# Kernel optimization log

Measured on AMD Instinct MI355X. Metric: run time of the kernel, lower is better.

The kernel has to match this reference:

```python
import jax, jax.numpy as jnp
import numpy as np

LAYER_SIZES = [1024, 1024, 1024, 1024, 1024, 1024, 512]
MAX_PATHS = 128
BATCH = 128
N_LAYERS = len(LAYER_SIZES) - 1


def setup_inputs() -> dict:
    key = jax.random.key(0)
    keys = jax.random.split(key, 1 + 2 * N_LAYERS)
    inp = {"x": jax.random.normal(keys[0], (BATCH, LAYER_SIZES[0]), dtype=jnp.float32)}
    for i in range(N_LAYERS):
        inp[f"W{i}"] = jax.random.normal(keys[1 + 2 * i], (LAYER_SIZES[i], LAYER_SIZES[i + 1]), dtype=jnp.float32) * 0.01
        inp[f"b{i}"] = jax.random.normal(keys[2 + 2 * i], (LAYER_SIZES[i + 1],), dtype=jnp.float32) * 0.01
    return inp


def _layer(data, W, b):
    # data: [B, in_feat, P] -> [B, out_feat, 3P]
    B, _, P = data.shape
    O = W.shape[1]
    pos = jnp.einsum('bfp,fo->bpo', data, W) + b          # [B, P, O]; neg branch is exactly -pos
    branches = jnp.stack([-pos, jnp.zeros_like(pos), pos], axis=-1)  # [B, P, O, 3]
    # transpose(1,2) then reshape: interleave branches per source path, matching torch
    return branches.transpose(0, 2, 1, 3).reshape(B, O, P * 3)


def _prune(data, keep):
    # keep top-`keep` paths by L2 norm over the feature dim
    norms = jnp.linalg.norm(data, axis=1)                 # [B, P]
    _, idx = jax.lax.top_k(norms, keep)                   # [B, keep]
    return jnp.take_along_axis(data, idx[:, None, :], axis=-1)


def _forward(x, Ws, bs):
    data = x[:, :, None]                                   # [B, F, 1]
    for i in range(N_LAYERS):
        data = _layer(data, Ws[i], bs[i])
        if i < N_LAYERS - 1:
            data = jnp.tanh(data)
        if data.shape[-1] > MAX_PATHS:
            data = _prune(data, MAX_PATHS)
    # collapse with 'max_abs': per (batch, feature) pick path with largest |value|
    idx = jnp.argmax(jnp.abs(data), axis=-1, keepdims=True)
    output = jnp.take_along_axis(data, idx, axis=-1).squeeze(-1)
    return output, data


def reference(x, W0, b0, W1, b1, W2, b2, W3, b3, W4, b4, W5, b5):
    Ws = [W0, W1, W2, W3, W4, W5]
    bs = [b0, b1, b2, b3, b4, b5]
    return _forward(x, Ws, bs)
```

## Files before the change

### kernel.cpp

```cpp
#include <hip/hip_runtime.h>
#include <math.h>


using s8v = __attribute__((ext_vector_type(8))) short;
using f4v = __attribute__((ext_vector_type(4))) float;

__device__ __forceinline__ float bf2f(short b) {
  unsigned u = ((unsigned)(unsigned short)b) << 16;
  return __builtin_bit_cast(float, u);
}
__device__ __forceinline__ short f2bf(float f) {
  unsigned u = __builtin_bit_cast(unsigned, f);
  u = (u + 0x7FFFu + ((u >> 16) & 1u)) >> 16;
  return (short)u;
}
__device__ __forceinline__ void split_store(float f, short* hi, short* lo) {
  short h = f2bf(f);
  *hi = h;
  *lo = f2bf(f - bf2f(h));
}

__global__ void __launch_bounds__(256)
packx_k(const float* __restrict__ x, short* __restrict__ hi,
        short* __restrict__ lo) {
  int i = (blockIdx.x * 256 + threadIdx.x) * 4;
  float4 v = *(const float4*)&x[i];
  short4 h, l;
  h.x = f2bf(v.x); l.x = f2bf(v.x - bf2f(h.x));
  h.y = f2bf(v.y); l.y = f2bf(v.y - bf2f(h.y));
  h.z = f2bf(v.z); l.z = f2bf(v.z - bf2f(h.z));
  h.w = f2bf(v.w); l.w = f2bf(v.w - bf2f(h.w));
  *(short4*)&hi[i] = h;
  *(short4*)&lo[i] = l;
}

struct TWArgs {
  const float* W[6];
  short* Th[6];
  short* Tl[6];
};
__global__ void __launch_bounds__(256)
transW_all(TWArgs a) {
  const int z = blockIdx.z;
  const int N = (z == 5) ? 512 : 1024;
  const int n0 = blockIdx.x * 64, k0 = blockIdx.y * 64;
  if (n0 >= N) return;
  const float* __restrict__ W = a.W[z];
  short* __restrict__ Th = a.Th[z];
  short* __restrict__ Tl = a.Tl[z];
  __shared__ float tile[64][65];
  const int t = threadIdx.x;
  const int r = t >> 4, c4 = (t & 15) * 4;
#pragma unroll
  for (int i = 0; i < 4; ++i) {
    int rr = r + 16 * i;
    float4 v = *(const float4*)&W[(size_t)(k0 + rr) * N + n0 + c4];
    tile[rr][c4 + 0] = v.x;
    tile[rr][c4 + 1] = v.y;
    tile[rr][c4 + 2] = v.z;
    tile[rr][c4 + 3] = v.w;
  }
  __syncthreads();
#pragma unroll
  for (int i = 0; i < 4; ++i) {
    int n = r + 16 * i;
    short4 h, l;
    float f0 = tile[c4 + 0][n], f1 = tile[c4 + 1][n];
    float f2 = tile[c4 + 2][n], f3 = tile[c4 + 3][n];
    h.x = f2bf(f0); l.x = f2bf(f0 - bf2f(h.x));
    h.y = f2bf(f1); l.y = f2bf(f1 - bf2f(h.y));
    h.z = f2bf(f2); l.z = f2bf(f2 - bf2f(h.z));
    h.w = f2bf(f3); l.w = f2bf(f3 - bf2f(h.w));
    size_t o = (size_t)(n0 + n) * 1024 + k0 + c4;
    *(short4*)&Th[o] = h;
    *(short4*)&Tl[o] = l;
  }
}

template <int MODE, int D, int KS>
__global__ void __launch_bounds__(256, 2)
mfma_gemm(const short* __restrict__ Ah, const short* __restrict__ Al,
          const short* __restrict__ Bh, const short* __restrict__ Bl,
          const float* __restrict__ bias, short* __restrict__ Oh,
          short* __restrict__ Ol, float* __restrict__ Of, int N, int Dn) {
  constexpr int KC = 1024 / KS;
  constexpr int BKP = 40;
  __shared__ short As_h[64 * BKP], As_l[64 * BKP];
  __shared__ short Bs_h[64 * BKP], Bs_l[64 * BKP];
  const int t = threadIdx.x;
  const int row0 = blockIdx.y * 64;
  const int col0 = blockIdx.x * 64;
  const int kb = blockIdx.z * KC;
  const int sr = t >> 2, sko = (t & 3) * 8;
  const short* Ahp = Ah + (size_t)(row0 + sr) * 1024 + kb + sko;
  const short* Alp = Al + (size_t)(row0 + sr) * 1024 + kb + sko;
  const short* Bhp = Bh + (size_t)(col0 + sr) * 1024 + kb + sko;
  const short* Blp = Bl + (size_t)(col0 + sr) * 1024 + kb + sko;
  const int w = t >> 6, lane = t & 63;
  const int l16 = lane & 15, q = lane >> 4;
  const int wm0 = (w & 1) * 32, wn0 = (w >> 1) * 32;
  const int abase = (wm0 + l16) * BKP + q * 8;
  const int bbase = (wn0 + l16) * BKP + q * 8;
  f4v acc[2][2];
#pragma unroll
  for (int i = 0; i < 2; ++i)
#pragma unroll
    for (int j = 0; j < 2; ++j) acc[i][j] = (f4v){0.f, 0.f, 0.f, 0.f};
  uint4 rah = *(const uint4*)(Ahp);
  uint4 ral = *(const uint4*)(Alp);
  uint4 rbh = *(const uint4*)(Bhp);
  uint4 rbl = *(const uint4*)(Blp);
  for (int k0 = 0; k0 < KC; k0 += 32) {
    __syncthreads();
    *(uint4*)&As_h[sr * BKP + sko] = rah;
    *(uint4*)&As_l[sr * BKP + sko] = ral;
    *(uint4*)&Bs_h[sr * BKP + sko] = rbh;
    *(uint4*)&Bs_l[sr * BKP + sko] = rbl;
    if (k0 + 32 < KC) {
      rah = *(const uint4*)(Ahp + k0 + 32);
      ral = *(const uint4*)(Alp + k0 + 32);
      rbh = *(const uint4*)(Bhp + k0 + 32);
      rbl = *(const uint4*)(Blp + k0 + 32);
    }
    __syncthreads();
    s8v ah[2], al[2], bh[2], bl[2];
#pragma unroll
    for (int mt = 0; mt < 2; ++mt) {
      ah[mt] = *(const s8v*)&As_h[abase + mt * 16 * BKP];
      al[mt] = *(const s8v*)&As_l[abase + mt * 16 * BKP];
    }
#pragma unroll
    for (int nt = 0; nt < 2; ++nt) {
      bh[nt] = *(const s8v*)&Bs_h[bbase + nt * 16 * BKP];
      bl[nt] = *(const s8v*)&Bs_l[bbase + nt * 16 * BKP];
    }
#pragma unroll
    for (int mt = 0; mt < 2; ++mt)
#pragma unroll
      for (int nt = 0; nt < 2; ++nt) {
        acc[mt][nt] = __builtin_amdgcn_mfma_f32_16x16x32_bf16(
            ah[mt], bh[nt], acc[mt][nt], 0, 0, 0);
        acc[mt][nt] = __builtin_amdgcn_mfma_f32_16x16x32_bf16(
            ah[mt], bl[nt], acc[mt][nt], 0, 0, 0);
        acc[mt][nt] = __builtin_amdgcn_mfma_f32_16x16x32_bf16(
            al[mt], bh[nt], acc[mt][nt], 0, 0, 0);
      }
  }
  const int R = (int)gridDim.y << 6;
#pragma unroll
  for (int nt = 0; nt < 2; ++nt) {
    int gcol = col0 + wn0 + nt * 16 + l16;
    float bc = (MODE == 1) ? bias[gcol] : 0.f;
#pragma unroll
    for (int mt = 0; mt < 2; ++mt) {
#pragma unroll
      for (int r = 0; r < 4; ++r) {
        float v = acc[mt][nt][r];
        int rr = row0 + wm0 + mt * 16 + q * 4 + r;
        if (MODE == 1) {
          int b = rr / D, u = rr - b * D;
          size_t ob = (size_t)(b * Dn) * N + gcol;
          size_t om = ob + (size_t)(1 + 2 * u) * N;
          size_t op = ob + (size_t)(2 + 2 * u) * N;
          split_store(tanhf(bc - v), &Oh[om], &Ol[om]);
          split_store(tanhf(bc + v), &Oh[op], &Ol[op]);
          if (u == 0) split_store(tanhf(bc), &Oh[ob], &Ol[ob]);
        } else if (MODE == 2) {
          Of[(size_t)rr * N + gcol] = v;
        } else {
          Of[((size_t)blockIdx.z * R + rr) * N + gcol] = v;
        }
      }
    }
  }
}

template <int KS>
__global__ void __launch_bounds__(256)
comb0_hl(const float* __restrict__ P, const float* __restrict__ bias,
         short* __restrict__ Oh, short* __restrict__ Ol, int R, int N) {
  int i = blockIdx.x * 256 + threadIdx.x;
  int n4 = N >> 2;
  int r = i / n4, c4 = (i - r * n4) * 4;
  float4 y = *(const float4*)&P[(size_t)r * N + c4];
  size_t stride = (size_t)R * N;
#pragma unroll
  for (int ks = 1; ks < KS; ++ks) {
    const float4 p = *(const float4*)&P[ks * stride + (size_t)r * N + c4];
    y.x += p.x; y.y += p.y; y.z += p.z; y.w += p.w;
  }
  float4 bc = *(const float4*)(bias + c4);
  float t0 = tanhf(bc.x + y.x), t1 = tanhf(bc.y + y.y);
  float t2 = tanhf(bc.z + y.z), t3 = tanhf(bc.w + y.w);
  short4 h, l;
  h.x = f2bf(t0); l.x = f2bf(t0 - bf2f(h.x));
  h.y = f2bf(t1); l.y = f2bf(t1 - bf2f(h.y));
  h.z = f2bf(t2); l.z = f2bf(t2 - bf2f(h.z));
  h.w = f2bf(t3); l.w = f2bf(t3 - bf2f(h.w));
  *(short4*)&Oh[(size_t)r * N + c4] = h;
  *(short4*)&Ol[(size_t)r * N + c4] = l;
}

template <int KS, int D>
__global__ void __launch_bounds__(256)
comb1_hl(const float* __restrict__ P, const float* __restrict__ bias,
         short* __restrict__ Oh, short* __restrict__ Ol, int R, int N,
         int Dn) {
  int i = blockIdx.x * 256 + threadIdx.x;
  int n4 = N >> 2;
  int r = i / n4, c4 = (i - r * n4) * 4;
  int b = r / D, u = r - b * D;
  float4 y = *(const float4*)&P[(size_t)r * N + c4];
  size_t stride = (size_t)R * N;
#pragma unroll
  for (int ks = 1; ks < KS; ++ks) {
    const float4 p = *(const float4*)&P[ks * stride + (size_t)r * N + c4];
    y.x += p.x; y.y += p.y; y.z += p.z; y.w += p.w;
  }
  float4 bc = *(const float4*)(bias + c4);
  size_t ob = (size_t)(b * Dn) * N + c4;
  size_t om = ob + (size_t)(1 + 2 * u) * N;
  size_t op = ob + (size_t)(2 + 2 * u) * N;
  {
    float t0 = tanhf(bc.x - y.x), t1 = tanhf(bc.y - y.y);
    float t2 = tanhf(bc.z - y.z), t3 = tanhf(bc.w - y.w);
    short4 h, l;
    h.x = f2bf(t0); l.x = f2bf(t0 - bf2f(h.x));
    h.y = f2bf(t1); l.y = f2bf(t1 - bf2f(h.y));
    h.z = f2bf(t2); l.z = f2bf(t2 - bf2f(h.z));
    h.w = f2bf(t3); l.w = f2bf(t3 - bf2f(h.w));
    *(short4*)&Oh[om] = h;
    *(short4*)&Ol[om] = l;
  }
  {
    float t0 = tanhf(bc.x + y.x), t1 = tanhf(bc.y + y.y);
    float t2 = tanhf(bc.z + y.z), t3 = tanhf(bc.w + y.w);
    short4 h, l;
    h.x = f2bf(t0); l.x = f2bf(t0 - bf2f(h.x));
    h.y = f2bf(t1); l.y = f2bf(t1 - bf2f(h.y));
    h.z = f2bf(t2); l.z = f2bf(t2 - bf2f(h.z));
    h.w = f2bf(t3); l.w = f2bf(t3 - bf2f(h.w));
    *(short4*)&Oh[op] = h;
    *(short4*)&Ol[op] = l;
  }
  if (u == 0) {
    float t0 = tanhf(bc.x), t1 = tanhf(bc.y);
    float t2 = tanhf(bc.z), t3 = tanhf(bc.w);
    short4 h, l;
    h.x = f2bf(t0); l.x = f2bf(t0 - bf2f(h.x));
    h.y = f2bf(t1); l.y = f2bf(t1 - bf2f(h.y));
    h.z = f2bf(t2); l.z = f2bf(t2 - bf2f(h.z));
    h.w = f2bf(t3); l.w = f2bf(t3 - bf2f(h.w));
    *(short4*)&Oh[ob] = h;
    *(short4*)&Ol[ob] = l;
  }
}

__global__ void __launch_bounds__(256)
rownorm_hl(const short* __restrict__ hi, const short* __restrict__ lo,
           float* __restrict__ ns) {
  int row = blockIdx.x;
  int t = threadIdx.x;
  size_t base = (size_t)row * 1024 + t * 4;
  short4 h = *(const short4*)&hi[base];
  short4 l = *(const short4*)&lo[base];
  float v0 = bf2f(h.x) + bf2f(l.x);
  float v1 = bf2f(h.y) + bf2f(l.y);
  float v2 = bf2f(h.z) + bf2f(l.z);
  float v3 = bf2f(h.w) + bf2f(l.w);
  float s = v0 * v0 + v1 * v1 + v2 * v2 + v3 * v3;
  __shared__ float red[256];
  red[t] = s;
  __syncthreads();
  for (int off = 128; off; off >>= 1) {
    if (t < off) red[t] += red[t + off];
    __syncthreads();
  }
  if (t == 0) ns[row] = red[0];
}

__global__ void __launch_bounds__(256)
prune4_k(const float* __restrict__ ns, int* __restrict__ kept4) {
  int b = blockIdx.x, t = threadIdx.x;
  __shared__ float nss[31];
  __shared__ float key[243];
  __shared__ int cls[243];
  if (t < 31) nss[t] = ns[b * 31 + t];
  __syncthreads();
  if (t < 243) {
    int j = t / 3, t4 = t - 3 * j;
    int d0 = j / 27, d1 = (j / 9) % 3, d2 = (j / 3) % 3, d3 = j % 3;
    int u = 0;
    u = (d0 == 1) ? 0 : (1 + 2 * u + (d0 == 2));
    u = (d1 == 1) ? 0 : (1 + 2 * u + (d1 == 2));
    u = (d2 == 1) ? 0 : (1 + 2 * u + (d2 == 2));
    u = (d3 == 1) ? 0 : (1 + 2 * u + (d3 == 2));
    cls[t] = u;
    key[t] = (t4 == 1) ? 0.f : nss[u];
  }
  __syncthreads();
  if (t < 243) {
    float k = key[t];
    int rank = 0;
    for (int e = 0; e < 243; ++e) {
      float ke = key[e];
      rank += (ke > k) || (ke == k && e < t);
    }
    if (rank < 128) {
      int t4 = t - 3 * (t / 3);
      kept4[b * 128 + rank] = (cls[t] << 1) | (t4 == 2 ? 1 : 0);
    }
  }
}

__global__ void __launch_bounds__(256)
stats5_k(const float* __restrict__ Y5, const float* __restrict__ b5,
         float* __restrict__ dotv, float* __restrict__ nrmv,
         float* __restrict__ nb5) {
  int row = blockIdx.x;
  int t = threadIdx.x;
  __shared__ float rd[256], rn[256];
  if (row < 3968) {
    const float* y = Y5 + (size_t)row * 512;
    float d = 0.f, n2 = 0.f;
    for (int o = t; o < 512; o += 256) {
      float v = y[o];
      d = fmaf(b5[o], v, d);
      n2 = fmaf(v, v, n2);
    }
    rd[t] = d;
    rn[t] = n2;
    __syncthreads();
    for (int off = 128; off; off >>= 1) {
      if (t < off) {
        rd[t] += rd[t + off];
        rn[t] += rn[t + off];
      }
      __syncthreads();
    }
    if (t == 0) {
      dotv[row] = rd[0];
      nrmv[row] = rn[0];
    }
  } else {
    float n2 = 0.f;
    for (int o = t; o < 512; o += 256) {
      float v = b5[o];
      n2 = fmaf(v, v, n2);
    }
    rn[t] = n2;
    __syncthreads();
    for (int off = 128; off; off >>= 1) {
      if (t < off) rn[t] += rn[t + off];
      __syncthreads();
    }
    if (t == 0) nb5[0] = rn[0];
  }
}

__global__ void __launch_bounds__(384)
prune5_k(const float* __restrict__ dotv, const float* __restrict__ nrmv,
         const float* __restrict__ nb5, const int* __restrict__ kept4,
         int* __restrict__ kept5) {
  int b = blockIdx.x, t = threadIdx.x;
  __shared__ float pns[128];
  __shared__ float key[384];
  if (t < 128) {
    int k4 = kept4[b * 128 + t];
    int c = k4 >> 1;
    float s = (k4 & 1) ? 1.f : -1.f;
    pns[t] = nb5[0] + nrmv[b * 31 + c] + s * 2.f * dotv[b * 31 + c];
  }
  __syncthreads();
  int m = t / 3, tt = t - 3 * m;
  key[t] = (tt == 1) ? 0.f : pns[m];
  __syncthreads();
  float k = key[t];
  int rank = 0;
  for (int e = 0; e < 384; ++e) {
    float ke = key[e];
    rank += (ke > k) || (ke == k && e < t);
  }
  if (rank < 128) kept5[b * 128 + rank] = (m << 1) | (tt == 2 ? 1 : 0);
}

__global__ void __launch_bounds__(256)
finalize_k(const float* __restrict__ Y5, const float* __restrict__ b5,
           const int* __restrict__ kept4, const int* __restrict__ kept5,
           float* __restrict__ out, float* __restrict__ dataout) {
  const int b = blockIdx.y;
  const int o0 = blockIdx.x * 64;
  __shared__ float Ys[31][65];
  __shared__ float bias_s[64];
  __shared__ float vt[64][130];
  __shared__ float ra[64][4];
  __shared__ float rv[64][4];
  const int t = threadIdx.x;
  for (int idx = t; idx < 31 * 64; idx += 256) {
    int c = idx >> 6, o = idx & 63;
    Ys[c][o] = Y5[((size_t)b * 31 + c) * 512 + o0 + o];
  }
  if (t < 64) bias_s[t] = b5[o0 + t];
  const int rr = t & 127, oh = t >> 7;
  int k5 = kept5[b * 128 + rr];
  int m = k5 >> 1;
  float sig = (k5 & 1) ? 1.f : -1.f;
  int k4 = kept4[b * 128 + m];
  int cc = k4 >> 1;
  float s4 = (k4 & 1) ? 1.f : -1.f;
  float afac = sig * s4;
  __syncthreads();
#pragma unroll
  for (int ol = 0; ol < 32; ++ol) {
    int o = oh * 32 + ol;
    float v = sig * bias_s[o] + afac * Ys[cc][o];
    dataout[((size_t)b * 512 + o0 + o) * 128 + rr] = v;
    vt[o][rr] = v;
  }
  __syncthreads();
  int o = t >> 2, q = t & 3;
  float bestv = vt[o][q * 32];
  float besta = fabsf(bestv);
  for (int i = 1; i < 32; ++i) {
    float v = vt[o][q * 32 + i];
    float a = fabsf(v);
    if (a > besta) {
      besta = a;
      bestv = v;
    }
  }
  ra[o][q] = besta;
  rv[o][q] = bestv;
  __syncthreads();
  if (t < 64) {
    float ba = ra[t][0], bv = rv[t][0];
#pragma unroll
    for (int qq = 1; qq < 4; ++qq) {
      if (ra[t][qq] > ba) {
        ba = ra[t][qq];
        bv = rv[t][qq];
      }
    }
    out[(size_t)b * 512 + o0 + t] = bv;
  }
}

extern "C" void kernel_launch(void* const* d_in, const int* in_sizes, int n_in,
                              void* d_out, int out_size, void* d_ws,
                              size_t ws_size, hipStream_t stream) {
  const float* x = (const float*)d_in[0];
  const float* Wt[6];
  const float* bs[6];
  for (int i = 0; i < 6; ++i) {
    Wt[i] = (const float*)d_in[1 + 2 * i];
    bs[i] = (const float*)d_in[2 + 2 * i];
  }
  char* base = (char*)d_ws;
  short* A0h = (short*)(base + 0);
  short* A0l = (short*)(base + 262144);
  short* Wh[6], *Wl[6];
  {
    size_t off = 524288;
    for (int i = 0; i < 6; ++i) {
      size_t sz = (i < 5) ? 2097152 : 1048576;
      Wh[i] = (short*)(base + off);
      Wl[i] = (short*)(base + off + sz);
      off += 2 * sz;
    }
  }
  short* C1h = (short*)(base + 23592960), *C1l = (short*)(base + 23855104);
  short* C2h = (short*)(base + 24117248), *C2l = (short*)(base + 24903680);
  short* C3h = (short*)(base + 25690112), *C3l = (short*)(base + 27525120);
  short* C4h = (short*)(base + 29360128), *C4l = (short*)(base + 33292288);
  short* C5h = (short*)(base + 524288);
  short* C5l = (short*)(base + 8912896);
  float* PA = (float*)(base + 29360128);
  float* PB = (float*)(base + 524288);
  float* Y5 = (float*)(base + 23592960);
  float* ns = (float*)(base + 37224448);
  float* dotv = (float*)(base + 37240320);
  float* nrmv = (float*)(base + 37256192);
  float* nb5 = (float*)(base + 37272064);
  int* kept4 = (int*)(base + 37272068);
  int* kept5 = (int*)(base + 37337604);
  float* outp = (float*)d_out;
  float* dataout = outp + 128 * 512;

  dim3 blk(256);
  packx_k<<<dim3(128), blk, 0, stream>>>(x, A0h, A0l);
  TWArgs twa;
  for (int i = 0; i < 6; ++i) {
    twa.W[i] = Wt[i];
    twa.Th[i] = Wh[i];
    twa.Tl[i] = Wl[i];
  }
  transW_all<<<dim3(16, 16, 6), blk, 0, stream>>>(twa);

  mfma_gemm<3, 1, 4><<<dim3(16, 2, 4), blk, 0, stream>>>(
      A0h, A0l, Wh[0], Wl[0], nullptr, nullptr, nullptr, PA, 1024, 0);
  comb0_hl<4><<<dim3(128), blk, 0, stream>>>(PA, bs[0], C1h, C1l, 128, 1024);
  mfma_gemm<3, 1, 4><<<dim3(16, 2, 4), blk, 0, stream>>>(
      C1h, C1l, Wh[1], Wl[1], nullptr, nullptr, nullptr, PA, 1024, 0);
  comb1_hl<4, 1><<<dim3(128), blk, 0, stream>>>(PA, bs[1], C2h, C2l, 128, 1024,
                                                3);
  mfma_gemm<3, 3, 4><<<dim3(16, 6, 4), blk, 0, stream>>>(
      C2h, C2l, Wh[2], Wl[2], nullptr, nullptr, nullptr, PA, 1024, 0);
  comb1_hl<4, 3><<<dim3(384), blk, 0, stream>>>(PA, bs[2], C3h, C3l, 384, 1024,
                                                7);
  mfma_gemm<3, 7, 2><<<dim3(16, 14, 2), blk, 0, stream>>>(
      C3h, C3l, Wh[3], Wl[3], nullptr, nullptr, nullptr, PB, 1024, 0);
  comb1_hl<2, 7><<<dim3(896), blk, 0, stream>>>(PB, bs[3], C4h, C4l, 896, 1024,
                                                15);
  mfma_gemm<1, 15, 1><<<dim3(16, 30), blk, 0, stream>>>(
      C4h, C4l, Wh[4], Wl[4], bs[4], C5h, C5l, nullptr, 1024, 31);
  rownorm_hl<<<dim3(3968), blk, 0, stream>>>(C5h, C5l, ns);
  prune4_k<<<dim3(128), blk, 0, stream>>>(ns, kept4);
  mfma_gemm<2, 31, 1><<<dim3(8, 62), blk, 0, stream>>>(
      C5h, C5l, Wh[5], Wl[5], nullptr, nullptr, nullptr, Y5, 512, 0);
  stats5_k<<<dim3(3969), blk, 0, stream>>>(Y5, bs[5], dotv, nrmv, nb5);
  prune5_k<<<dim3(128), dim3(384), 0, stream>>>(dotv, nrmv, nb5, kept4, kept5);
  finalize_k<<<dim3(8, 128), blk, 0, stream>>>(Y5, bs[5], kept4, kept5, outp,
                                               dataout);
}
```

Before: 238.5 us.

## Fuse row-norm and stats reductions into GEMM epilogues and merge x packing

Drops the rownorm_hl and stats5_k kernels by computing squared norms and bias dot products inside the GEMM epilogues, using wave shuffles and global atomicAdd into a buffer that is zeroed beforehand. The x bf16 split and that zeroing move into the weight-transpose launch as an extra z slice, and the bias norm is now computed inside prune5_k. This removes several launches and a re-read of the layer-5 activations and Y5, at the cost of atomic traffic and floating-point sums whose order is no longer fixed, which could change near-tie top-k choices.

```diff
diff --git a/kernel.cpp b/kernel.cpp
--- a/kernel.cpp
+++ b/kernel.cpp
@@ -20,28 +20,36 @@
   *lo = f2bf(f - bf2f(h));
 }
 
-__global__ void __launch_bounds__(256)
-packx_k(const float* __restrict__ x, short* __restrict__ hi,
-        short* __restrict__ lo) {
-  int i = (blockIdx.x * 256 + threadIdx.x) * 4;
-  float4 v = *(const float4*)&x[i];
-  short4 h, l;
-  h.x = f2bf(v.x); l.x = f2bf(v.x - bf2f(h.x));
-  h.y = f2bf(v.y); l.y = f2bf(v.y - bf2f(h.y));
-  h.z = f2bf(v.z); l.z = f2bf(v.z - bf2f(h.z));
-  h.w = f2bf(v.w); l.w = f2bf(v.w - bf2f(h.w));
-  *(short4*)&hi[i] = h;
-  *(short4*)&lo[i] = l;
-}
-
 struct TWArgs {
   const float* W[6];
   short* Th[6];
   short* Tl[6];
+  const float* x;
+  short* A0h;
+  short* A0l;
+  float* zone;
 };
 __global__ void __launch_bounds__(256)
 transW_all(TWArgs a) {
   const int z = blockIdx.z;
+  const int t = threadIdx.x;
+  if (z == 6) {
+    int bid = blockIdx.y * 16 + blockIdx.x;
+    if (bid < 128) {
+      int i = (bid * 256 + t) * 4;
+      float4 v = *(const float4*)&a.x[i];
+      short4 h, l;
+      h.x = f2bf(v.x); l.x = f2bf(v.x - bf2f(h.x));
+      h.y = f2bf(v.y); l.y = f2bf(v.y - bf2f(h.y));
+      h.z = f2bf(v.z); l.z = f2bf(v.z - bf2f(h.z));
+      h.w = f2bf(v.w); l.w = f2bf(v.w - bf2f(h.w));
+      *(short4*)&a.A0h[i] = h;
+      *(short4*)&a.A0l[i] = l;
+    } else if (bid < 176) {
+      a.zone[(bid - 128) * 256 + t] = 0.f;
+    }
+    return;
+  }
   const int N = (z == 5) ? 512 : 1024;
   const int n0 = blockIdx.x * 64, k0 = blockIdx.y * 64;
   if (n0 >= N) return;
@@ -49,7 +57,6 @@
   short* __restrict__ Th = a.Th[z];
   short* __restrict__ Tl = a.Tl[z];
   __shared__ float tile[64][65];
-  const int t = threadIdx.x;
   const int r = t >> 4, c4 = (t & 15) * 4;
 #pragma unroll
   for (int i = 0; i < 4; ++i) {
@@ -77,12 +84,14 @@
   }
 }
 
-template <int MODE, int D, int KS>
+template <int EPI, int D, int KS>
 __global__ void __launch_bounds__(256, 2)
 mfma_gemm(const short* __restrict__ Ah, const short* __restrict__ Al,
           const short* __restrict__ Bh, const short* __restrict__ Bl,
           const float* __restrict__ bias, short* __restrict__ Oh,
-          short* __restrict__ Ol, float* __restrict__ Of, int N, int Dn) {
+          short* __restrict__ Ol, float* __restrict__ Of,
+          float* __restrict__ ns, float* __restrict__ dotv,
+          float* __restrict__ nrmv, int N, int Dn) {
   constexpr int KC = 1024 / KS;
   constexpr int BKP = 40;
   __shared__ short As_h[64 * BKP], As_l[64 * BKP];
@@ -146,32 +155,100 @@
             al[mt], bh[nt], acc[mt][nt], 0, 0, 0);
       }
   }
-  const int R = (int)gridDim.y << 6;
-#pragma unroll
-  for (int nt = 0; nt < 2; ++nt) {
-    int gcol = col0 + wn0 + nt * 16 + l16;
-    float bc = (MODE == 1) ? bias[gcol] : 0.f;
-#pragma unroll
-    for (int mt = 0; mt < 2; ++mt) {
+
+  if constexpr (EPI == 0) {
+    const int R = (int)gridDim.y << 6;
+#pragma unroll
+    for (int nt = 0; nt < 2; ++nt) {
+      int gcol = col0 + wn0 + nt * 16 + l16;
+#pragma unroll
+      for (int mt = 0; mt < 2; ++mt)
+#pragma unroll
+        for (int r = 0; r < 4; ++r) {
+          int rr = row0 + wm0 + mt * 16 + q * 4 + r;
+          Of[((size_t)blockIdx.z * R + rr) * N + gcol] = acc[mt][nt][r];
+        }
+    }
+  } else if constexpr (EPI == 1) {
+    float bcr[2];
+    int gc[2];
+#pragma unroll
+    for (int nt = 0; nt < 2; ++nt) {
+      gc[nt] = col0 + wn0 + nt * 16 + l16;
+      bcr[nt] = bias[gc[nt]];
+    }
+#pragma unroll
+    for (int mt = 0; mt < 2; ++mt)
 #pragma unroll
       for (int r = 0; r < 4; ++r) {
-        float v = acc[mt][nt][r];
         int rr = row0 + wm0 + mt * 16 + q * 4 + r;
-        if (MODE == 1) {
-          int b = rr / D, u = rr - b * D;
-          size_t ob = (size_t)(b * Dn) * N + gcol;
-          size_t om = ob + (size_t)(1 + 2 * u) * N;
-          size_t op = ob + (size_t)(2 + 2 * u) * N;
-          split_store(tanhf(bc - v), &Oh[om], &Ol[om]);
-          split_store(tanhf(bc + v), &Oh[op], &Ol[op]);
-          if (u == 0) split_store(tanhf(bc), &Oh[ob], &Ol[ob]);
-        } else if (MODE == 2) {
-          Of[(size_t)rr * N + gcol] = v;
-        } else {
-          Of[((size_t)blockIdx.z * R + rr) * N + gcol] = v;
+        int b = rr / D, u = rr - b * D;
+        size_t ob = (size_t)(b * Dn) * (size_t)N;
+        size_t om = ob + (size_t)(1 + 2 * u) * N;
+        size_t op = ob + (size_t)(2 + 2 * u) * N;
+        float sm = 0.f, sp = 0.f;
+#pragma unroll
+        for (int nt = 0; nt < 2; ++nt) {
+          float v = acc[mt][nt][r];
+          float tm = tanhf(bcr[nt] - v), tp = tanhf(bcr[nt] + v);
+          split_store(tm, &Oh[om + gc[nt]], &Ol[om + gc[nt]]);
+          split_store(tp, &Oh[op + gc[nt]], &Ol[op + gc[nt]]);
+          sm = fmaf(tm, tm, sm);
+          sp = fmaf(tp, tp, sp);
+        }
+#pragma unroll
+        for (int msk = 1; msk < 16; msk <<= 1) {
+          sm += __shfl_xor(sm, msk);
+          sp += __shfl_xor(sp, msk);
+        }
+        if (l16 == 0) {
+          atomicAdd(&ns[b * Dn + 1 + 2 * u], sm);
+          atomicAdd(&ns[b * Dn + 2 + 2 * u], sp);
+        }
+        if (u == 0) {
+          float sz = 0.f;
+#pragma unroll
+          for (int nt = 0; nt < 2; ++nt) {
+            float tz = tanhf(bcr[nt]);
+            split_store(tz, &Oh[ob + gc[nt]], &Ol[ob + gc[nt]]);
+            sz = fmaf(tz, tz, sz);
+          }
+#pragma unroll
+          for (int msk = 1; msk < 16; msk <<= 1) sz += __shfl_xor(sz, msk);
+          if (l16 == 0) atomicAdd(&ns[b * Dn], sz);
         }
       }
-    }
+  } else {
+    float b5r[2];
+    int gc[2];
+#pragma unroll
+    for (int nt = 0; nt < 2; ++nt) {
+      gc[nt] = col0 + wn0 + nt * 16 + l16;
+      b5r[nt] = bias[gc[nt]];
+    }
+#pragma unroll
+    for (int mt = 0; mt < 2; ++mt)
+#pragma unroll
+      for (int r = 0; r < 4; ++r) {
+        int rr = row0 + wm0 + mt * 16 + q * 4 + r;
+        float nr = 0.f, dt = 0.f;
+#pragma unroll
+        for (int nt = 0; nt < 2; ++nt) {
+          float v = acc[mt][nt][r];
+          Of[(size_t)rr * N + gc[nt]] = v;
+          nr = fmaf(v, v, nr);
+          dt = fmaf(v, b5r[nt], dt);
+        }
+#pragma unroll
+        for (int msk = 1; msk < 16; msk <<= 1) {
+          nr += __shfl_xor(nr, msk);
+          dt += __shfl_xor(dt, msk);
+        }
+        if (l16 == 0) {
+          atomicAdd(&nrmv[rr], nr);
+          atomicAdd(&dotv[rr], dt);
+        }
+      }
   }
 }
 
@@ -257,29 +334,6 @@
 }
 
 __global__ void __launch_bounds__(256)
-rownorm_hl(const short* __restrict__ hi, const short* __restrict__ lo,
-           float* __restrict__ ns) {
-  int row = blockIdx.x;
-  int t = threadIdx.x;
-  size_t base = (size_t)row * 1024 + t * 4;
-  short4 h = *(const short4*)&hi[base];
-  short4 l = *(const short4*)&lo[base];
-  float v0 = bf2f(h.x) + bf2f(l.x);
-  float v1 = bf2f(h.y) + bf2f(l.y);
-  float v2 = bf2f(h.z) + bf2f(l.z);
-  float v3 = bf2f(h.w) + bf2f(l.w);
-  float s = v0 * v0 + v1 * v1 + v2 * v2 + v3 * v3;
-  __shared__ float red[256];
-  red[t] = s;
-  __syncthreads();
-  for (int off = 128; off; off >>= 1) {
-    if (t < off) red[t] += red[t + off];
-    __syncthreads();
-  }
-  if (t == 0) ns[row] = red[0];
-}
-
-__global__ void __launch_bounds__(256)
 prune4_k(const float* __restrict__ ns, int* __restrict__ kept4) {
   int b = blockIdx.x, t = threadIdx.x;
   __shared__ float nss[31];
@@ -313,63 +367,40 @@
   }
 }
 
-__global__ void __launch_bounds__(256)
-stats5_k(const float* __restrict__ Y5, const float* __restrict__ b5,
-         float* __restrict__ dotv, float* __restrict__ nrmv,
-         float* __restrict__ nb5) {
-  int row = blockIdx.x;
-  int t = threadIdx.x;
-  __shared__ float rd[256], rn[256];
-  if (row < 3968) {
-    const float* y = Y5 + (size_t)row * 512;
-    float d = 0.f, n2 = 0.f;
-    for (int o = t; o < 512; o += 256) {
-      float v = y[o];
-      d = fmaf(b5[o], v, d);
-      n2 = fmaf(v, v, n2);
-    }
-    rd[t] = d;
-    rn[t] = n2;
-    __syncthreads();
-    for (int off = 128; off; off >>= 1) {
-      if (t < off) {
-        rd[t] += rd[t + off];
-        rn[t] += rn[t + off];
-      }
-      __syncthreads();
-    }
-    if (t == 0) {
-      dotv[row] = rd[0];
-      nrmv[row] = rn[0];
-    }
-  } else {
-    float n2 = 0.f;
-    for (int o = t; o < 512; o += 256) {
-      float v = b5[o];
-      n2 = fmaf(v, v, n2);
-    }
-    rn[t] = n2;
-    __syncthreads();
-    for (int off = 128; off; off >>= 1) {
-      if (t < off) rn[t] += rn[t + off];
-      __syncthreads();
-    }
-    if (t == 0) nb5[0] = rn[0];
-  }
-}
-
 __global__ void __launch_bounds__(384)
 prune5_k(const float* __restrict__ dotv, const float* __restrict__ nrmv,
-         const float* __restrict__ nb5, const int* __restrict__ kept4,
+         const float* __restrict__ b5, const int* __restrict__ kept4,
          int* __restrict__ kept5) {
   int b = blockIdx.x, t = threadIdx.x;
+  __shared__ float red[384];
   __shared__ float pns[128];
   __shared__ float key[384];
+  float p = 0.f;
+  for (int o = t; o < 512; o += 384) p = fmaf(b5[o], b5[o], p);
+  red[t] = p;
+  __syncthreads();
+  if (t < 128) red[t] = red[t] + red[t + 128] + red[t + 256];
+  __syncthreads();
+  if (t < 64) red[t] += red[t + 64];
+  __syncthreads();
+  if (t < 32) red[t] += red[t + 32];
+  __syncthreads();
+  if (t < 16) red[t] += red[t + 16];
+  __syncthreads();
+  if (t < 8) red[t] += red[t + 8];
+  __syncthreads();
+  if (t < 4) red[t] += red[t + 4];
+  __syncthreads();
+  if (t < 2) red[t] += red[t + 2];
+  __syncthreads();
+  if (t == 0) red[0] += red[1];
+  __syncthreads();
+  float nb5 = red[0];
   if (t < 128) {
     int k4 = kept4[b * 128 + t];
     int c = k4 >> 1;
     float s = (k4 & 1) ? 1.f : -1.f;
-    pns[t] = nb5[0] + nrmv[b * 31 + c] + s * 2.f * dotv[b * 31 + c];
+    pns[t] = nb5 + nrmv[b * 31 + c] + s * 2.f * dotv[b * 31 + c];
   }
   __syncthreads();
   int m = t / 3, tt = t - 3 * m;
@@ -478,47 +509,54 @@
   float* PB = (float*)(base + 524288);
   float* Y5 = (float*)(base + 23592960);
   float* ns = (float*)(base + 37224448);
-  float* dotv = (float*)(base + 37240320);
-  float* nrmv = (float*)(base + 37256192);
-  float* nb5 = (float*)(base + 37272064);
-  int* kept4 = (int*)(base + 37272068);
-  int* kept5 = (int*)(base + 37337604);
+  float* dotv = ns + 3968;
+  float* nrmv = dotv + 3968;
+  int* kept4 = (int*)(base + 37273600);
+  int* kept5 = (int*)(base + 37339136);
   float* outp = (float*)d_out;
   float* dataout = outp + 128 * 512;
 
   dim3 blk(256);
-  packx_k<<<dim3(128), blk, 0, stream>>>(x, A0h, A0l);
   TWArgs twa;
   for (int i = 0; i < 6; ++i) {
     twa.W[i] = Wt[i];
     twa.Th[i] = Wh[i];
     twa.Tl[i] = Wl[i];
   }
-  transW_all<<<dim3(16, 16, 6), blk, 0, stream>>>(twa);
-
-  mfma_gemm<3, 1, 4><<<dim3(16, 2, 4), blk, 0, stream>>>(
-      A0h, A0l, Wh[0], Wl[0], nullptr, nullptr, nullptr, PA, 1024, 0);
+  twa.x = x;
+  twa.A0h = A0h;
+  twa.A0l = A0l;
+  twa.zone = ns;
+  transW_all<<<dim3(16, 16, 7), blk, 0, stream>>>(twa);
+
+  mfma_gemm<0, 1, 4><<<dim3(16, 2, 4), blk, 0, stream>>>(
+      A0h, A0l, Wh[0], Wl[0], nullptr, nullptr, nullptr, PA, nullptr, nullptr,
+      nullptr, 1024, 1);
   comb0_hl<4><<<dim3(128), blk, 0, stream>>>(PA, bs[0], C1h, C1l, 128, 1024);
-  mfma_gemm<3, 1, 4><<<dim3(16, 2, 4), blk, 0, stream>>>(
-      C1h, C1l, Wh[1], Wl[1], nullptr, nullptr, nullptr, PA, 1024, 0);
+  mfma_gemm<0, 1, 4><<<dim3(16, 2, 4), blk, 0, stream>>>(
+      C1h, C1l, Wh[1], Wl[1], nullptr, nullptr, nullptr, PA, nullptr, nullptr,
+      nullptr, 1024, 3);
   comb1_hl<4, 1><<<dim3(128), blk, 0, stream>>>(PA, bs[1], C2h, C2l, 128, 1024,
                                                 3);
-  mfma_gemm<3, 3, 4><<<dim3(16, 6, 4), blk, 0, stream>>>(
-      C2h, C2l, Wh[2], Wl[2], nullptr, nullptr, nullptr, PA, 1024, 0);
+  mfma_gemm<0, 3, 4><<<dim3(16, 6, 4), blk, 0, stream>>>(
+      C2h, C2l, Wh[2], Wl[2], nullptr, nullptr, nullptr, PA, nullptr, nullptr,
+      nullptr, 1024, 7);
   comb1_hl<4, 3><<<dim3(384), blk, 0, stream>>>(PA, bs[2], C3h, C3l, 384, 1024,
                                                 7);
-  mfma_gemm<3, 7, 2><<<dim3(16, 14, 2), blk, 0, stream>>>(
-      C3h, C3l, Wh[3], Wl[3], nullptr, nullptr, nullptr, PB, 1024, 0);
+  mfma_gemm<0, 7, 2><<<dim3(16, 14, 2), blk, 0, stream>>>(
+      C3h, C3l, Wh[3], Wl[3], nullptr, nullptr, nullptr, PB, nullptr, nullptr,
+      nullptr, 1024, 15);
   comb1_hl<2, 7><<<dim3(896), blk, 0, stream>>>(PB, bs[3], C4h, C4l, 896, 1024,
                                                 15);
   mfma_gemm<1, 15, 1><<<dim3(16, 30), blk, 0, stream>>>(
-      C4h, C4l, Wh[4], Wl[4], bs[4], C5h, C5l, nullptr, 1024, 31);
-  rownorm_hl<<<dim3(3968), blk, 0, stream>>>(C5h, C5l, ns);
+      C4h, C4l, Wh[4], Wl[4], bs[4], C5h, C5l, nullptr, ns, nullptr, nullptr,
+      1024, 31);
   prune4_k<<<dim3(128), blk, 0, stream>>>(ns, kept4);
   mfma_gemm<2, 31, 1><<<dim3(8, 62), blk, 0, stream>>>(
-      C5h, C5l, Wh[5], Wl[5], nullptr, nullptr, nullptr, Y5, 512, 0);
-  stats5_k<<<dim3(3969), blk, 0, stream>>>(Y5, bs[5], dotv, nrmv, nb5);
-  prune5_k<<<dim3(128), dim3(384), 0, stream>>>(dotv, nrmv, nb5, kept4, kept5);
+      C5h, C5l, Wh[5], Wl[5], bs[5], nullptr, nullptr, Y5, nullptr, dotv, nrmv,
+      512, 0);
+  prune5_k<<<dim3(128), dim3(384), 0, stream>>>(dotv, nrmv, bs[5], kept4,
+                                                kept5);
   finalize_k<<<dim3(8, 128), blk, 0, stream>>>(Y5, bs[5], kept4, kept5, outp,
                                                dataout);
 }
```

Result: slower. 246.5 us (+3.3%).
